# Performance work log

Measured on AMD Instinct MI355X. Metric: run time of the kernel, lower is better.

Reference implementation:

```python
import jax, jax.numpy as jnp
import numpy as np

B, S, E, H = 512, 100, 256, 256
C_EXPLORE = 10.0  # tanh_exploration


def setup_inputs() -> dict:
    key = jax.random.key(0)
    ks = jax.random.split(key, 22)
    sH = 1.0 / np.sqrt(H)
    sE = 1.0 / np.sqrt(E)
    u = lambda k, shp, s: jax.random.uniform(k, shp, minval=-s, maxval=s, dtype=jnp.float32)
    return {
        "inputs": jax.random.uniform(ks[0], (B, 2, S), dtype=jnp.float32),  # 2D coords in [0,1)
        "emb": u(ks[1], (2, E), sE),
        "enc_Wih": u(ks[2], (4 * H, E), sH), "enc_Whh": u(ks[3], (4 * H, H), sH),
        "enc_bih": u(ks[4], (4 * H,), sH), "enc_bhh": u(ks[5], (4 * H,), sH),
        "dec_Wih": u(ks[6], (4 * H, E), sH), "dec_Whh": u(ks[7], (4 * H, H), sH),
        "dec_bih": u(ks[8], (4 * H,), sH), "dec_bhh": u(ks[9], (4 * H,), sH),
        "g_Wq": u(ks[10], (H, H), sH), "g_bq": u(ks[11], (H,), sH),
        "g_Wr": u(ks[12], (H, H), sH), "g_br": u(ks[13], (H,), sH),
        "g_V": u(ks[14], (H,), sH),
        "p_Wq": u(ks[15], (H, H), sH), "p_bq": u(ks[16], (H,), sH),
        "p_Wr": u(ks[17], (H, H), sH), "p_br": u(ks[18], (H,), sH),
        "p_V": u(ks[19], (H,), sH),
        "start": u(ks[20], (E,), sE),
    }


def _lstm_cell(x, h, c, Wih, Whh, bih, bhh):
    # torch LSTM gate order: input, forget, cell, output
    g = x @ Wih.T + h @ Whh.T + bih + bhh
    i, f, gg, o = jnp.split(g, 4, axis=-1)
    c = jax.nn.sigmoid(f) * c + jax.nn.sigmoid(i) * jnp.tanh(gg)
    return jax.nn.sigmoid(o) * jnp.tanh(c), c


def _forward(inputs, emb, enc_Wih, enc_Whh, enc_bih, enc_bhh,
             dec_Wih, dec_Whh, dec_bih, dec_bhh,
             g_Wq, g_bq, g_Wr, g_br, g_V,
             p_Wq, p_bq, p_Wr, p_br, p_V, start):
    # GraphEmbedding: per-position bmm([B,1,2],[B,2,E]) == single einsum
    embedded = jnp.einsum('bcs,ce->bse', inputs, emb)  # [B,S,E]

    h0 = jnp.zeros((B, H), jnp.float32)
    c0 = jnp.zeros((B, H), jnp.float32)

    def enc_step(carry, x_t):
        h, c = carry
        h, c = _lstm_cell(x_t, h, c, enc_Wih, enc_Whh, enc_bih, enc_bhh)
        return (h, c), h

    (h, c), outs = jax.lax.scan(enc_step, (h0, c0), embedded.transpose(1, 0, 2))
    enc = outs.transpose(1, 0, 2)  # encoder_outputs [B,S,H]

    # Conv1d(k=1) projection of encoder outputs is step-invariant: precompute once.
    ref_g = jnp.einsum('bsh,oh->bso', enc, g_Wr) + g_br  # [B,S,H]
    ref_p = jnp.einsum('bsh,oh->bso', enc, p_Wr) + p_br  # [B,S,H]

    keys = jax.random.split(jax.random.key(1), S)
    arange_b = jnp.arange(B)

    def attn(q, ref_proj, Wq, bq, V):
        qq = q @ Wq.T + bq  # [B,H]
        return jnp.einsum('h,bsh->bs', V, jnp.tanh(qq[:, None, :] + ref_proj))

    def step(carry, k):
        h, c, mask, idxs, valid, dec_in = carry
        h, c = _lstm_cell(dec_in, h, c, dec_Wih, dec_Whh, dec_bih, dec_bhh)
        # apply_mask_to_logits: mask grows by idxs only after first selection
        mask = jnp.where(valid, mask.at[arange_b, idxs].set(True), mask)
        # glimpse (n_glimpses = 1, use_tanh=False)
        lg = jnp.where(mask, -jnp.inf, attn(h, ref_g, g_Wq, g_bq, g_V))
        q = jnp.einsum('bsh,bs->bh', enc, jax.nn.softmax(lg, axis=-1))
        # pointer (use_tanh=True, C=10)
        lp = C_EXPLORE * jnp.tanh(attn(q, ref_p, p_Wq, p_bq, p_V))
        lp = jnp.where(mask, -jnp.inf, lp)
        probs = jax.nn.softmax(lp, axis=-1)
        idxs = jax.random.categorical(k, lp)  # multinomial(probs, 1)
        dec_in = embedded[arange_b, idxs]
        return (h, c, mask, idxs, jnp.array(True), dec_in), (probs, idxs)

    init = (h, c, jnp.zeros((B, S), bool), jnp.zeros((B,), jnp.int32),
            jnp.array(False), jnp.broadcast_to(start, (B, E)))
    _, (probs, idxs) = jax.lax.scan(step, init, keys)
    return probs, idxs  # [S,B,S] float, [S,B] int


def reference(inputs, emb, enc_Wih, enc_Whh, enc_bih, enc_bhh,
              dec_Wih, dec_Whh, dec_bih, dec_bhh,
              g_Wq, g_bq, g_Wr, g_br, g_V,
              p_Wq, p_bq, p_Wr, p_br, p_V, start):
    return _forward(inputs, emb, enc_Wih, enc_Whh, enc_bih, enc_bhh,
                    dec_Wih, dec_Whh, dec_bih, dec_bhh,
                    g_Wq, g_bq, g_Wr, g_br, g_V,
                    p_Wq, p_bq, p_Wr, p_br, p_V, start)
```

## Files before the change

### kernel.cpp

```cpp
#include <hip/hip_runtime.h>
#include <cstdint>
#include <math.h>

#define B_ 512
#define S_ 100
#define E_ 256
#define H_ 256

__device__ __forceinline__ float sigmoidf_(float x){ return 1.0f/(1.0f+expf(-x)); }

__device__ __forceinline__ void threefry2x32_(uint32_t k0, uint32_t k1,
                                              uint32_t c0, uint32_t c1,
                                              uint32_t& o0, uint32_t& o1){
  uint32_t ks2 = k0 ^ k1 ^ 0x1BD11BDAu;
  uint32_t x0 = c0 + k0, x1 = c1 + k1;
#define ROT_(x,d) (((x)<<(d))|((x)>>(32-(d))))
#define RND_(r) { x0 += x1; x1 = ROT_(x1,(r)); x1 ^= x0; }
  RND_(13) RND_(15) RND_(26) RND_(6)  x0 += k1;  x1 += ks2 + 1u;
  RND_(17) RND_(29) RND_(16) RND_(24) x0 += ks2; x1 += k0  + 2u;
  RND_(13) RND_(15) RND_(26) RND_(6)  x0 += k0;  x1 += k1  + 3u;
  RND_(17) RND_(29) RND_(16) RND_(24) x0 += k1;  x1 += ks2 + 4u;
  RND_(13) RND_(15) RND_(26) RND_(6)  x0 += ks2; x1 += k0  + 5u;
#undef RND_
#undef ROT_
  o0 = x0; o1 = x1;
}

__device__ __forceinline__ float gumbel_bits_(uint32_t bits){
  const float tiny = 1.175494350822287508e-38f;
  float u = __uint_as_float((bits >> 9) | 0x3f800000u) - 1.0f;
  u = fmaxf(tiny, u + tiny);
  return -logf(-logf(u));
}

__device__ __forceinline__ float wsum_(float v){
  #pragma unroll
  for (int d = 32; d > 0; d >>= 1) v += __shfl_xor(v, d, 64);
  return v;
}
__device__ __forceinline__ float wmax_(float v){
  #pragma unroll
  for (int d = 32; d > 0; d >>= 1) v = fmaxf(v, __shfl_xor(v, d, 64));
  return v;
}

__global__ __launch_bounds__(256) void prep_wt(const float* __restrict__ Wih,
                                               const float* __restrict__ Whh,
                                               float* __restrict__ Wt){
  int idx = blockIdx.x*256 + threadIdx.x;
  int k = idx >> 10, j = idx & 1023;
  Wt[idx] = (k < 256) ? Wih[j*256 + k] : Whh[j*256 + (k-256)];
}
__global__ __launch_bounds__(256) void prep_bias(const float* __restrict__ b1,
                                                 const float* __restrict__ b2,
                                                 float* __restrict__ o, int n){
  int i = blockIdx.x*256 + threadIdx.x; if (i < n) o[i] = b1[i] + b2[i];
}
__global__ __launch_bounds__(256) void transpose256(const float* __restrict__ src,
                                                    float* __restrict__ dst){
  int idx = blockIdx.x*256 + threadIdx.x;
  int r = idx >> 8, cc = idx & 255;
  dst[idx] = src[cc*256 + r];
}
__global__ __launch_bounds__(256) void init_state(float* __restrict__ h, float* __restrict__ c,
                                                  int* __restrict__ mask, int* __restrict__ sel){
  int i = blockIdx.x*256 + threadIdx.x;
  if (i < B_*H_) { h[i] = 0.f; c[i] = 0.f; }
  if (i < B_*S_) mask[i] = 0;
  if (i < B_)    sel[i]  = -1;
}

__global__ __launch_bounds__(256) void lstm_step_kernel(
    const float* __restrict__ Wt,
    const float* __restrict__ bsum,
    const float* __restrict__ coords,
    const float* __restrict__ emb,
    const float* __restrict__ start,
    const int*   __restrict__ sel,
    float* __restrict__ h, float* __restrict__ c,
    float* __restrict__ enc_out,
    int t, int mode)
{
  const int tid = threadIdx.x;
  const int b0  = blockIdx.x * 4;
  __shared__ float xh[4][512];

  const float e0 = emb[tid], e1 = emb[256 + tid];
  #pragma unroll
  for (int r = 0; r < 4; ++r) {
    const int b = b0 + r;
    float xv;
    if (mode == 0) {
      xv = coords[b*200 + t]*e0 + coords[b*200 + 100 + t]*e1;
    } else {
      int s = sel[b];
      if (s < 0) xv = start[tid];
      else       xv = coords[b*200 + s]*e0 + coords[b*200 + 100 + s]*e1;
    }
    xh[r][tid]       = xv;
    xh[r][256 + tid] = h[b*256 + tid];
  }
  __syncthreads();

  float acc[4][4] = {};
  #pragma unroll 4
  for (int k = 0; k < 512; ++k) {
    const float* wr = Wt + (size_t)k*1024 + tid;
    const float w0 = wr[0], w1 = wr[256], w2 = wr[512], w3 = wr[768];
    #pragma unroll
    for (int r = 0; r < 4; ++r) {
      const float xv = xh[r][k];
      acc[r][0] += xv*w0; acc[r][1] += xv*w1;
      acc[r][2] += xv*w2; acc[r][3] += xv*w3;
    }
  }

  const float bi_ = bsum[tid], bf_ = bsum[256+tid], bg_ = bsum[512+tid], bo_ = bsum[768+tid];
  #pragma unroll
  for (int r = 0; r < 4; ++r) {
    const int b = b0 + r;
    const float gi = acc[r][0] + bi_;
    const float gf = acc[r][1] + bf_;
    const float gg = acc[r][2] + bg_;
    const float go = acc[r][3] + bo_;
    const float cN = sigmoidf_(gf)*c[b*256+tid] + sigmoidf_(gi)*tanhf(gg);
    const float hN = sigmoidf_(go)*tanhf(cN);
    c[b*256 + tid] = cN;
    h[b*256 + tid] = hN;
    if (mode == 0) enc_out[((size_t)b*S_ + t)*H_ + tid] = hN;
  }
}

__global__ __launch_bounds__(256) void gemm_ref(
    const float* __restrict__ A, const float* __restrict__ Bt,
    const float* __restrict__ bias, float* __restrict__ C)
{
  const int tid = threadIdx.x;
  const int m0 = blockIdx.x * 128, n0 = blockIdx.y * 128;
  __shared__ float As[8][128];
  __shared__ float Bs[8][128];
  float acc[8][8] = {};
  const int tx = tid & 15, ty = tid >> 4;

  for (int k0 = 0; k0 < 256; k0 += 8) {
    {
      const int row = tid >> 1, q = tid & 1;
      const float4 av = *(const float4*)(A + (size_t)(m0+row)*256 + k0 + q*4);
      As[q*4+0][row] = av.x; As[q*4+1][row] = av.y;
      As[q*4+2][row] = av.z; As[q*4+3][row] = av.w;
    }
    {
      const int kk = tid >> 5, nq = tid & 31;
      *(float4*)(&Bs[kk][nq*4]) = *(const float4*)(Bt + (size_t)(k0+kk)*256 + n0 + nq*4);
    }
    __syncthreads();
    #pragma unroll
    for (int k = 0; k < 8; ++k) {
      float a[8], bb[8];
      *(float4*)&a[0]  = *(const float4*)&As[k][ty*8];
      *(float4*)&a[4]  = *(const float4*)&As[k][ty*8+4];
      *(float4*)&bb[0] = *(const float4*)&Bs[k][tx*8];
      *(float4*)&bb[4] = *(const float4*)&Bs[k][tx*8+4];
      #pragma unroll
      for (int i = 0; i < 8; ++i)
        #pragma unroll
        for (int j = 0; j < 8; ++j)
          acc[i][j] += a[i]*bb[j];
    }
    __syncthreads();
  }
  #pragma unroll
  for (int i = 0; i < 8; ++i) {
    const int m = m0 + ty*8 + i;
    #pragma unroll
    for (int j = 0; j < 8; j += 4) {
      const int n = n0 + tx*8 + j;
      float4 o;
      o.x = acc[i][j  ] + bias[n  ];
      o.y = acc[i][j+1] + bias[n+1];
      o.z = acc[i][j+2] + bias[n+2];
      o.w = acc[i][j+3] + bias[n+3];
      *(float4*)(C + (size_t)m*256 + n) = o;
    }
  }
}

__global__ __launch_bounds__(256) void attn_step(
    const float* __restrict__ h, const float* __restrict__ enc,
    const float* __restrict__ ref_g, const float* __restrict__ ref_p,
    const float* __restrict__ gWqT, const float* __restrict__ g_bq, const float* __restrict__ g_V,
    const float* __restrict__ pWqT, const float* __restrict__ p_bq, const float* __restrict__ p_V,
    int* __restrict__ mask, int* __restrict__ sel,
    float* __restrict__ probs_out, float* __restrict__ idx_out, int t)
{
  const int b    = blockIdx.x;
  const int tid  = threadIdx.x;
  const int lane = tid & 63;
  const int wv   = tid >> 6;

  __shared__ float hs[256], qqs[256], qs[256], pqs[256];
  __shared__ float gVs[256], pVs[256];
  __shared__ float lg[128], alpha[128], lp[128];

  hs[tid]  = h[b*256 + tid];
  gVs[tid] = g_V[tid];
  pVs[tid] = p_V[tid];
  __syncthreads();

  {
    float a = g_bq[tid];
    for (int k = 0; k < 256; ++k) a += hs[k] * gWqT[k*256 + tid];
    qqs[tid] = a;
  }
  __syncthreads();

  {
    const float* rg = ref_g + (size_t)b*S_*H_;
    const int* mk = mask + b*S_;
    for (int is = 0; is < 25; ++is) {
      const int s = is*4 + wv;
      float p = 0.f;
      #pragma unroll
      for (int j = 0; j < 4; ++j) {
        const int hh = lane + 64*j;
        p += gVs[hh] * tanhf(qqs[hh] + rg[s*256 + hh]);
      }
      p = wsum_(p);
      if (lane == 0) lg[s] = mk[s] ? -INFINITY : p;
    }
  }
  __syncthreads();

  if (wv == 0) {
    const float v0 = lg[lane];
    const float v1 = (lane + 64 < S_) ? lg[lane + 64] : -INFINITY;
    const float m  = wmax_(fmaxf(v0, v1));
    const float e0 = expf(v0 - m);
    const float e1 = (lane + 64 < S_) ? expf(v1 - m) : 0.f;
    const float sm = wsum_(e0 + e1);
    alpha[lane] = e0 / sm;
    if (lane + 64 < S_) alpha[lane + 64] = e1 / sm;
  }
  __syncthreads();

  {
    const float* eb = enc + (size_t)b*S_*H_;
    float a = 0.f;
    for (int s = 0; s < S_; ++s) a += alpha[s] * eb[s*256 + tid];
    qs[tid] = a;
  }
  __syncthreads();

  {
    float a = p_bq[tid];
    for (int k = 0; k < 256; ++k) a += qs[k] * pWqT[k*256 + tid];
    pqs[tid] = a;
  }
  __syncthreads();

  {
    const float* rp = ref_p + (size_t)b*S_*H_;
    const int* mk = mask + b*S_;
    for (int is = 0; is < 25; ++is) {
      const int s = is*4 + wv;
      float p = 0.f;
      #pragma unroll
      for (int j = 0; j < 4; ++j) {
        const int hh = lane + 64*j;
        p += pVs[hh] * tanhf(pqs[hh] + rp[s*256 + hh]);
      }
      p = wsum_(p);
      if (lane == 0) {
        const float v = 10.0f * tanhf(p);
        lp[s] = mk[s] ? -INFINITY : v;
      }
    }
  }
  __syncthreads();

  if (wv == 0) {
    const float v0 = lp[lane];
    const float v1 = (lane + 64 < S_) ? lp[lane + 64] : -INFINITY;
    const float m  = wmax_(fmaxf(v0, v1));
    const float e0 = expf(v0 - m);
    const float e1 = (lane + 64 < S_) ? expf(v1 - m) : 0.f;
    const float sm = wsum_(e0 + e1);
    float* po = probs_out + ((size_t)t*B_ + b)*S_;
    po[lane] = e0 / sm;
    if (lane + 64 < S_) po[lane + 64] = e1 / sm;

    uint32_t k0, k1; threefry2x32_(0u, 1u, 0u, (uint32_t)t, k0, k1);
    uint32_t r0, r1;
    threefry2x32_(k0, k1, 0u, (uint32_t)(b*S_ + lane), r0, r1);
    float z0 = v0 + gumbel_bits_(r0 ^ r1);
    float z1 = -INFINITY;
    if (lane + 64 < S_) {
      uint32_t q0, q1;
      threefry2x32_(k0, k1, 0u, (uint32_t)(b*S_ + lane + 64), q0, q1);
      z1 = v1 + gumbel_bits_(q0 ^ q1);
    }
    float bv; int bi;
    if (z1 > z0) { bv = z1; bi = lane + 64; } else { bv = z0; bi = lane; }
    #pragma unroll
    for (int d = 32; d > 0; d >>= 1) {
      const float ov = __shfl_xor(bv, d, 64);
      const int   oi = __shfl_xor(bi, d, 64);
      if (ov > bv || (ov == bv && oi < bi)) { bv = ov; bi = oi; }
    }
    if (lane == 0) {
      idx_out[t*B_ + b] = (float)bi;
      sel[b] = bi;
      mask[b*S_ + bi] = 1;
    }
  }
}

extern "C" void kernel_launch(void* const* d_in, const int* in_sizes, int n_in,
                              void* d_out, int out_size, void* d_ws, size_t ws_size,
                              hipStream_t stream) {
  (void)in_sizes; (void)n_in; (void)out_size; (void)ws_size;
  const float* inputs = (const float*)d_in[0];
  const float* emb    = (const float*)d_in[1];
  const float* eWih   = (const float*)d_in[2];
  const float* eWhh   = (const float*)d_in[3];
  const float* ebih   = (const float*)d_in[4];
  const float* ebhh   = (const float*)d_in[5];
  const float* dWih   = (const float*)d_in[6];
  const float* dWhh   = (const float*)d_in[7];
  const float* dbih   = (const float*)d_in[8];
  const float* dbhh   = (const float*)d_in[9];
  const float* gWq    = (const float*)d_in[10];
  const float* gbq    = (const float*)d_in[11];
  const float* gWr    = (const float*)d_in[12];
  const float* gbr    = (const float*)d_in[13];
  const float* gV     = (const float*)d_in[14];
  const float* pWq    = (const float*)d_in[15];
  const float* pbq    = (const float*)d_in[16];
  const float* pWr    = (const float*)d_in[17];
  const float* pbr    = (const float*)d_in[18];
  const float* pV     = (const float*)d_in[19];
  const float* start  = (const float*)d_in[20];

  float* ws = (float*)d_ws;
  size_t o = 0;
  float* WtE  = ws + o; o += (size_t)512*1024;
  float* WtD  = ws + o; o += (size_t)512*1024;
  float* bE   = ws + o; o += 1024;
  float* bD   = ws + o; o += 1024;
  float* gWqT = ws + o; o += 65536;
  float* pWqT = ws + o; o += 65536;
  float* gWrT = ws + o; o += 65536;
  float* pWrT = ws + o; o += 65536;
  float* enc  = ws + o; o += (size_t)B_*S_*H_;
  float* refg = ws + o; o += (size_t)B_*S_*H_;
  float* refp = ws + o; o += (size_t)B_*S_*H_;
  float* h    = ws + o; o += (size_t)B_*H_;
  float* c    = ws + o; o += (size_t)B_*H_;
  int* mask   = (int*)(ws + o); o += (size_t)B_*S_;
  int* sel    = (int*)(ws + o); o += B_;

  float* probs = (float*)d_out;
  float* idxo  = probs + (size_t)S_*B_*S_;

  prep_wt<<<2048,256,0,stream>>>(eWih, eWhh, WtE);
  prep_wt<<<2048,256,0,stream>>>(dWih, dWhh, WtD);
  prep_bias<<<4,256,0,stream>>>(ebih, ebhh, bE, 1024);
  prep_bias<<<4,256,0,stream>>>(dbih, dbhh, bD, 1024);
  transpose256<<<256,256,0,stream>>>(gWq, gWqT);
  transpose256<<<256,256,0,stream>>>(pWq, pWqT);
  transpose256<<<256,256,0,stream>>>(gWr, gWrT);
  transpose256<<<256,256,0,stream>>>(pWr, pWrT);
  init_state<<<512,256,0,stream>>>(h, c, mask, sel);

  for (int t = 0; t < S_; ++t)
    lstm_step_kernel<<<128,256,0,stream>>>(WtE, bE, inputs, emb, nullptr, nullptr,
                                           h, c, enc, t, 0);

  gemm_ref<<<dim3(400,2),256,0,stream>>>(enc, gWrT, gbr, refg);
  gemm_ref<<<dim3(400,2),256,0,stream>>>(enc, pWrT, pbr, refp);

  for (int t = 0; t < S_; ++t) {
    lstm_step_kernel<<<128,256,0,stream>>>(WtD, bD, inputs, emb, start, sel,
                                           h, c, nullptr, t, 1);
    attn_step<<<512,256,0,stream>>>(h, enc, refg, refp,
                                    gWqT, gbq, gV, pWqT, pbq, pV,
                                    mask, sel, probs, idxo, t);
  }
}
```

Before: 18.85 ms.

## Split attention into batched matvec kernels and retile LSTM step with interleaved gate weights

The LSTM step kernel is retiled so each block handles 8 batch rows and 64 hidden units, reading gate-interleaved weights as float4 and using double-buffered h to avoid the read/write hazard once multiple blocks share a batch row. The fused per-batch attention kernel, which recomputed query projections with a full 256x256 weight read per batch element, is split into separate matvec kernels that process 4 batch rows per block plus glimpse and pointer kernels. This cuts redundant weight traffic and raises parallelism, at the cost of more kernel launches per decode step and extra global round-trips for the intermediate vectors.

```diff
diff --git a/kernel.cpp b/kernel.cpp
--- a/kernel.cpp
+++ b/kernel.cpp
@@ -44,17 +44,22 @@
   return v;
 }
 
-__global__ __launch_bounds__(256) void prep_wt(const float* __restrict__ Wih,
+__global__ __launch_bounds__(256) void prep_w4(const float* __restrict__ Wih,
                                                const float* __restrict__ Whh,
-                                               float* __restrict__ Wt){
+                                               float* __restrict__ W4){
   int idx = blockIdx.x*256 + threadIdx.x;
-  int k = idx >> 10, j = idx & 1023;
-  Wt[idx] = (k < 256) ? Wih[j*256 + k] : Whh[j*256 + (k-256)];
-}
-__global__ __launch_bounds__(256) void prep_bias(const float* __restrict__ b1,
-                                                 const float* __restrict__ b2,
-                                                 float* __restrict__ o, int n){
-  int i = blockIdx.x*256 + threadIdx.x; if (i < n) o[i] = b1[i] + b2[i];
+  int g = idx & 3, u = (idx >> 2) & 255, k = idx >> 10;
+  int row = g*256 + u;
+  W4[idx] = (k < 256) ? Wih[row*256 + k] : Whh[row*256 + (k-256)];
+}
+__global__ __launch_bounds__(256) void prep_b4(const float* __restrict__ b1,
+                                               const float* __restrict__ b2,
+                                               float* __restrict__ o){
+  int idx = blockIdx.x*256 + threadIdx.x;
+  if (idx < 1024) {
+    int g = idx & 3, u = idx >> 2;
+    o[idx] = b1[g*256 + u] + b2[g*256 + u];
+  }
 }
 __global__ __launch_bounds__(256) void transpose256(const float* __restrict__ src,
                                                     float* __restrict__ dst){
@@ -70,64 +75,206 @@
   if (i < B_)    sel[i]  = -1;
 }
 
-__global__ __launch_bounds__(256) void lstm_step_kernel(
-    const float* __restrict__ Wt,
-    const float* __restrict__ bsum,
+__global__ __launch_bounds__(256) void lstm_step2(
+    const float* __restrict__ W4,
+    const float* __restrict__ b4,
     const float* __restrict__ coords,
     const float* __restrict__ emb,
     const float* __restrict__ start,
     const int*   __restrict__ sel,
-    float* __restrict__ h, float* __restrict__ c,
+    const float* __restrict__ hr,
+    float* __restrict__ hw,
+    float* __restrict__ cst,
     float* __restrict__ enc_out,
     int t, int mode)
 {
   const int tid = threadIdx.x;
-  const int b0  = blockIdx.x * 4;
-  __shared__ float xh[4][512];
-
-  const float e0 = emb[tid], e1 = emb[256 + tid];
-  #pragma unroll
-  for (int r = 0; r < 4; ++r) {
-    const int b = b0 + r;
-    float xv;
-    if (mode == 0) {
-      xv = coords[b*200 + t]*e0 + coords[b*200 + 100 + t]*e1;
+  const int uu  = tid & 63;
+  const int rg  = tid >> 6;
+  const int b0  = (blockIdx.x >> 2) * 8;
+  const int u0  = (blockIdx.x & 3) * 64;
+  __shared__ float Xs[512*8];
+
+  for (int i = tid; i < 4096; i += 256) {
+    const int k = i >> 3, r = i & 7, b = b0 + r;
+    float v;
+    if (k < 256) {
+      if (mode == 0) {
+        v = coords[b*200 + t]*emb[k] + coords[b*200 + 100 + t]*emb[256 + k];
+      } else {
+        const int s = sel[b];
+        if (s < 0) v = start[k];
+        else       v = coords[b*200 + s]*emb[k] + coords[b*200 + 100 + s]*emb[256 + k];
+      }
     } else {
-      int s = sel[b];
-      if (s < 0) xv = start[tid];
-      else       xv = coords[b*200 + s]*e0 + coords[b*200 + 100 + s]*e1;
-    }
-    xh[r][tid]       = xv;
-    xh[r][256 + tid] = h[b*256 + tid];
-  }
-  __syncthreads();
-
-  float acc[4][4] = {};
+      v = hr[b*256 + (k - 256)];
+    }
+    Xs[i] = v;
+  }
+  __syncthreads();
+
+  float a0x=0.f,a0y=0.f,a0z=0.f,a0w=0.f, a1x=0.f,a1y=0.f,a1z=0.f,a1w=0.f;
+  const float* wp = W4 + (size_t)(u0 + uu)*4;
   #pragma unroll 4
   for (int k = 0; k < 512; ++k) {
-    const float* wr = Wt + (size_t)k*1024 + tid;
-    const float w0 = wr[0], w1 = wr[256], w2 = wr[512], w3 = wr[768];
+    const float4 w = *(const float4*)(wp + (size_t)k*1024);
+    const float2 x = *(const float2*)(Xs + k*8 + rg*2);
+    a0x += x.x*w.x; a0y += x.x*w.y; a0z += x.x*w.z; a0w += x.x*w.w;
+    a1x += x.y*w.x; a1y += x.y*w.y; a1z += x.y*w.z; a1w += x.y*w.w;
+  }
+
+  const float4 bb = *(const float4*)(b4 + (u0 + uu)*4);
+  const int u = u0 + uu;
+  {
+    const int b = b0 + rg*2;
+    const float gi = a0x + bb.x, gf = a0y + bb.y, gg = a0z + bb.z, go = a0w + bb.w;
+    const float cN = sigmoidf_(gf)*cst[b*256+u] + sigmoidf_(gi)*tanhf(gg);
+    const float hN = sigmoidf_(go)*tanhf(cN);
+    cst[b*256+u] = cN; hw[b*256+u] = hN;
+    if (mode == 0) enc_out[((size_t)b*S_ + t)*H_ + u] = hN;
+  }
+  {
+    const int b = b0 + rg*2 + 1;
+    const float gi = a1x + bb.x, gf = a1y + bb.y, gg = a1z + bb.z, go = a1w + bb.w;
+    const float cN = sigmoidf_(gf)*cst[b*256+u] + sigmoidf_(gi)*tanhf(gg);
+    const float hN = sigmoidf_(go)*tanhf(cN);
+    cst[b*256+u] = cN; hw[b*256+u] = hN;
+    if (mode == 0) enc_out[((size_t)b*S_ + t)*H_ + u] = hN;
+  }
+}
+
+__global__ __launch_bounds__(256) void matvec_bias(
+    const float* __restrict__ X, const float* __restrict__ WT,
+    const float* __restrict__ bias, float* __restrict__ out)
+{
+  const int tid = threadIdx.x;
+  const int b0 = blockIdx.x * 4;
+  __shared__ float Xs[1024];
+  for (int i = tid; i < 1024; i += 256)
+    Xs[i] = X[(b0 + (i & 3))*256 + (i >> 2)];
+  __syncthreads();
+  float a0 = bias[tid];
+  float a1 = a0, a2 = a0, a3 = a0;
+  #pragma unroll 4
+  for (int k = 0; k < 256; ++k) {
+    const float w = WT[k*256 + tid];
+    const float4 x = *(const float4*)(Xs + k*4);
+    a0 += x.x*w; a1 += x.y*w; a2 += x.z*w; a3 += x.w*w;
+  }
+  out[(b0+0)*256 + tid] = a0;
+  out[(b0+1)*256 + tid] = a1;
+  out[(b0+2)*256 + tid] = a2;
+  out[(b0+3)*256 + tid] = a3;
+}
+
+__global__ __launch_bounds__(256) void glimpse_step(
+    const float* __restrict__ qqIn, const float* __restrict__ enc,
+    const float* __restrict__ ref_g, const float* __restrict__ g_V,
+    const int* __restrict__ mask, float* __restrict__ qOut)
+{
+  const int b = blockIdx.x, tid = threadIdx.x, lane = tid & 63, wv = tid >> 6;
+  __shared__ float qqs[256], gVs[256], lg[128], alpha[128];
+  qqs[tid] = qqIn[b*256 + tid];
+  gVs[tid] = g_V[tid];
+  __syncthreads();
+
+  const float* rg = ref_g + (size_t)b*S_*H_;
+  const int* mk = mask + b*S_;
+  for (int is = 0; is < 25; ++is) {
+    const int s = is*4 + wv;
+    float p = 0.f;
     #pragma unroll
-    for (int r = 0; r < 4; ++r) {
-      const float xv = xh[r][k];
-      acc[r][0] += xv*w0; acc[r][1] += xv*w1;
-      acc[r][2] += xv*w2; acc[r][3] += xv*w3;
-    }
-  }
-
-  const float bi_ = bsum[tid], bf_ = bsum[256+tid], bg_ = bsum[512+tid], bo_ = bsum[768+tid];
-  #pragma unroll
-  for (int r = 0; r < 4; ++r) {
-    const int b = b0 + r;
-    const float gi = acc[r][0] + bi_;
-    const float gf = acc[r][1] + bf_;
-    const float gg = acc[r][2] + bg_;
-    const float go = acc[r][3] + bo_;
-    const float cN = sigmoidf_(gf)*c[b*256+tid] + sigmoidf_(gi)*tanhf(gg);
-    const float hN = sigmoidf_(go)*tanhf(cN);
-    c[b*256 + tid] = cN;
-    h[b*256 + tid] = hN;
-    if (mode == 0) enc_out[((size_t)b*S_ + t)*H_ + tid] = hN;
+    for (int j = 0; j < 4; ++j) {
+      const int hh = lane + 64*j;
+      p += gVs[hh] * tanhf(qqs[hh] + rg[s*256 + hh]);
+    }
+    p = wsum_(p);
+    if (lane == 0) lg[s] = mk[s] ? -INFINITY : p;
+  }
+  __syncthreads();
+
+  if (wv == 0) {
+    const float v0 = lg[lane];
+    const float v1 = (lane + 64 < S_) ? lg[lane + 64] : -INFINITY;
+    const float m  = wmax_(fmaxf(v0, v1));
+    const float e0 = expf(v0 - m);
+    const float e1 = (lane + 64 < S_) ? expf(v1 - m) : 0.f;
+    const float sm = wsum_(e0 + e1);
+    alpha[lane] = e0 / sm;
+    if (lane + 64 < S_) alpha[lane + 64] = e1 / sm;
+  }
+  __syncthreads();
+
+  const float* eb = enc + (size_t)b*S_*H_;
+  float a = 0.f;
+  for (int s = 0; s < S_; ++s) a += alpha[s] * eb[s*256 + tid];
+  qOut[b*256 + tid] = a;
+}
+
+__global__ __launch_bounds__(256) void pointer_step(
+    const float* __restrict__ pqIn, const float* __restrict__ ref_p,
+    const float* __restrict__ p_V,
+    int* __restrict__ mask, int* __restrict__ sel,
+    float* __restrict__ probs_out, float* __restrict__ idx_out, int t)
+{
+  const int b = blockIdx.x, tid = threadIdx.x, lane = tid & 63, wv = tid >> 6;
+  __shared__ float pqs[256], pVs[256], lp[128];
+  pqs[tid] = pqIn[b*256 + tid];
+  pVs[tid] = p_V[tid];
+  __syncthreads();
+
+  const float* rp = ref_p + (size_t)b*S_*H_;
+  const int* mk = mask + b*S_;
+  for (int is = 0; is < 25; ++is) {
+    const int s = is*4 + wv;
+    float p = 0.f;
+    #pragma unroll
+    for (int j = 0; j < 4; ++j) {
+      const int hh = lane + 64*j;
+      p += pVs[hh] * tanhf(pqs[hh] + rp[s*256 + hh]);
+    }
+    p = wsum_(p);
+    if (lane == 0) {
+      const float v = 10.0f * tanhf(p);
+      lp[s] = mk[s] ? -INFINITY : v;
+    }
+  }
+  __syncthreads();
+
+  if (wv == 0) {
+    const float v0 = lp[lane];
+    const float v1 = (lane + 64 < S_) ? lp[lane + 64] : -INFINITY;
+    const float m  = wmax_(fmaxf(v0, v1));
+    const float e0 = expf(v0 - m);
+    const float e1 = (lane + 64 < S_) ? expf(v1 - m) : 0.f;
+    const float sm = wsum_(e0 + e1);
+    float* po = probs_out + ((size_t)t*B_ + b)*S_;
+    po[lane] = e0 / sm;
+    if (lane + 64 < S_) po[lane + 64] = e1 / sm;
+
+    uint32_t k0, k1; threefry2x32_(0u, 1u, 0u, (uint32_t)t, k0, k1);
+    uint32_t r0, r1;
+    threefry2x32_(k0, k1, 0u, (uint32_t)(b*S_ + lane), r0, r1);
+    float z0 = v0 + gumbel_bits_(r0 ^ r1);
+    float z1 = -INFINITY;
+    if (lane + 64 < S_) {
+      uint32_t q0, q1;
+      threefry2x32_(k0, k1, 0u, (uint32_t)(b*S_ + lane + 64), q0, q1);
+      z1 = v1 + gumbel_bits_(q0 ^ q1);
+    }
+    float bv; int bi;
+    if (z1 > z0) { bv = z1; bi = lane + 64; } else { bv = z0; bi = lane; }
+    #pragma unroll
+    for (int d = 32; d > 0; d >>= 1) {
+      const float ov = __shfl_xor(bv, d, 64);
+      const int   oi = __shfl_xor(bi, d, 64);
+      if (ov > bv || (ov == bv && oi < bi)) { bv = ov; bi = oi; }
+    }
+    if (lane == 0) {
+      idx_out[t*B_ + b] = (float)bi;
+      sel[b] = bi;
+      mask[b*S_ + bi] = 1;
+    }
   }
 }
 
@@ -181,136 +328,6 @@
       o.z = acc[i][j+2] + bias[n+2];
       o.w = acc[i][j+3] + bias[n+3];
       *(float4*)(C + (size_t)m*256 + n) = o;
-    }
-  }
-}
-
-__global__ __launch_bounds__(256) void attn_step(
-    const float* __restrict__ h, const float* __restrict__ enc,
-    const float* __restrict__ ref_g, const float* __restrict__ ref_p,
-    const float* __restrict__ gWqT, const float* __restrict__ g_bq, const float* __restrict__ g_V,
-    const float* __restrict__ pWqT, const float* __restrict__ p_bq, const float* __restrict__ p_V,
-    int* __restrict__ mask, int* __restrict__ sel,
-    float* __restrict__ probs_out, float* __restrict__ idx_out, int t)
-{
-  const int b    = blockIdx.x;
-  const int tid  = threadIdx.x;
-  const int lane = tid & 63;
-  const int wv   = tid >> 6;
-
-  __shared__ float hs[256], qqs[256], qs[256], pqs[256];
-  __shared__ float gVs[256], pVs[256];
-  __shared__ float lg[128], alpha[128], lp[128];
-
-  hs[tid]  = h[b*256 + tid];
-  gVs[tid] = g_V[tid];
-  pVs[tid] = p_V[tid];
-  __syncthreads();
-
-  {
-    float a = g_bq[tid];
-    for (int k = 0; k < 256; ++k) a += hs[k] * gWqT[k*256 + tid];
-    qqs[tid] = a;
-  }
-  __syncthreads();
-
-  {
-    const float* rg = ref_g + (size_t)b*S_*H_;
-    const int* mk = mask + b*S_;
-    for (int is = 0; is < 25; ++is) {
-      const int s = is*4 + wv;
-      float p = 0.f;
-      #pragma unroll
-      for (int j = 0; j < 4; ++j) {
-        const int hh = lane + 64*j;
-        p += gVs[hh] * tanhf(qqs[hh] + rg[s*256 + hh]);
-      }
-      p = wsum_(p);
-      if (lane == 0) lg[s] = mk[s] ? -INFINITY : p;
-    }
-  }
-  __syncthreads();
-
-  if (wv == 0) {
-    const float v0 = lg[lane];
-    const float v1 = (lane + 64 < S_) ? lg[lane + 64] : -INFINITY;
-    const float m  = wmax_(fmaxf(v0, v1));
-    const float e0 = expf(v0 - m);
-    const float e1 = (lane + 64 < S_) ? expf(v1 - m) : 0.f;
-    const float sm = wsum_(e0 + e1);
-    alpha[lane] = e0 / sm;
-    if (lane + 64 < S_) alpha[lane + 64] = e1 / sm;
-  }
-  __syncthreads();
-
-  {
-    const float* eb = enc + (size_t)b*S_*H_;
-    float a = 0.f;
-    for (int s = 0; s < S_; ++s) a += alpha[s] * eb[s*256 + tid];
-    qs[tid] = a;
-  }
-  __syncthreads();
-
-  {
-    float a = p_bq[tid];
-    for (int k = 0; k < 256; ++k) a += qs[k] * pWqT[k*256 + tid];
-    pqs[tid] = a;
-  }
-  __syncthreads();
-
-  {
-    const float* rp = ref_p + (size_t)b*S_*H_;
-    const int* mk = mask + b*S_;
-    for (int is = 0; is < 25; ++is) {
-      const int s = is*4 + wv;
-      float p = 0.f;
-      #pragma unroll
-      for (int j = 0; j < 4; ++j) {
-        const int hh = lane + 64*j;
-        p += pVs[hh] * tanhf(pqs[hh] + rp[s*256 + hh]);
-      }
-      p = wsum_(p);
-      if (lane == 0) {
-        const float v = 10.0f * tanhf(p);
-        lp[s] = mk[s] ? -INFINITY : v;
-      }
-    }
-  }
-  __syncthreads();
-
-  if (wv == 0) {
-    const float v0 = lp[lane];
-    const float v1 = (lane + 64 < S_) ? lp[lane + 64] : -INFINITY;
-    const float m  = wmax_(fmaxf(v0, v1));
-    const float e0 = expf(v0 - m);
-    const float e1 = (lane + 64 < S_) ? expf(v1 - m) : 0.f;
-    const float sm = wsum_(e0 + e1);
-    float* po = probs_out + ((size_t)t*B_ + b)*S_;
-    po[lane] = e0 / sm;
-    if (lane + 64 < S_) po[lane + 64] = e1 / sm;
-
-    uint32_t k0, k1; threefry2x32_(0u, 1u, 0u, (uint32_t)t, k0, k1);
-    uint32_t r0, r1;
-    threefry2x32_(k0, k1, 0u, (uint32_t)(b*S_ + lane), r0, r1);
-    float z0 = v0 + gumbel_bits_(r0 ^ r1);
-    float z1 = -INFINITY;
-    if (lane + 64 < S_) {
-      uint32_t q0, q1;
-      threefry2x32_(k0, k1, 0u, (uint32_t)(b*S_ + lane + 64), q0, q1);
-      z1 = v1 + gumbel_bits_(q0 ^ q1);
-    }
-    float bv; int bi;
-    if (z1 > z0) { bv = z1; bi = lane + 64; } else { bv = z0; bi = lane; }
-    #pragma unroll
-    for (int d = 32; d > 0; d >>= 1) {
-      const float ov = __shfl_xor(bv, d, 64);
-      const int   oi = __shfl_xor(bi, d, 64);
-      if (ov > bv || (ov == bv && oi < bi)) { bv = ov; bi = oi; }
-    }
-    if (lane == 0) {
-      idx_out[t*B_ + b] = (float)bi;
-      sel[b] = bi;
-      mask[b*S_ + bi] = 1;
     }
   }
 }
@@ -343,10 +360,10 @@
 
   float* ws = (float*)d_ws;
   size_t o = 0;
-  float* WtE  = ws + o; o += (size_t)512*1024;
-  float* WtD  = ws + o; o += (size_t)512*1024;
-  float* bE   = ws + o; o += 1024;
-  float* bD   = ws + o; o += 1024;
+  float* W4E  = ws + o; o += (size_t)512*1024;
+  float* W4D  = ws + o; o += (size_t)512*1024;
+  float* b4E  = ws + o; o += 1024;
+  float* b4D  = ws + o; o += 1024;
   float* gWqT = ws + o; o += 65536;
   float* pWqT = ws + o; o += 65536;
   float* gWrT = ws + o; o += 65536;
@@ -354,36 +371,47 @@
   float* enc  = ws + o; o += (size_t)B_*S_*H_;
   float* refg = ws + o; o += (size_t)B_*S_*H_;
   float* refp = ws + o; o += (size_t)B_*S_*H_;
-  float* h    = ws + o; o += (size_t)B_*H_;
+  float* h0   = ws + o; o += (size_t)B_*H_;
+  float* h1   = ws + o; o += (size_t)B_*H_;
   float* c    = ws + o; o += (size_t)B_*H_;
+  float* qq   = ws + o; o += (size_t)B_*H_;
+  float* qb   = ws + o; o += (size_t)B_*H_;
+  float* pq   = ws + o; o += (size_t)B_*H_;
   int* mask   = (int*)(ws + o); o += (size_t)B_*S_;
   int* sel    = (int*)(ws + o); o += B_;
 
   float* probs = (float*)d_out;
   float* idxo  = probs + (size_t)S_*B_*S_;
 
-  prep_wt<<<2048,256,0,stream>>>(eWih, eWhh, WtE);
-  prep_wt<<<2048,256,0,stream>>>(dWih, dWhh, WtD);
-  prep_bias<<<4,256,0,stream>>>(ebih, ebhh, bE, 1024);
-  prep_bias<<<4,256,0,stream>>>(dbih, dbhh, bD, 1024);
+  float* hpp[2] = {h0, h1};
+  int p = 0;
+
+  prep_w4<<<2048,256,0,stream>>>(eWih, eWhh, W4E);
+  prep_w4<<<2048,256,0,stream>>>(dWih, dWhh, W4D);
+  prep_b4<<<4,256,0,stream>>>(ebih, ebhh, b4E);
+  prep_b4<<<4,256,0,stream>>>(dbih, dbhh, b4D);
   transpose256<<<256,256,0,stream>>>(gWq, gWqT);
   transpose256<<<256,256,0,stream>>>(pWq, pWqT);
   transpose256<<<256,256,0,stream>>>(gWr, gWrT);
   transpose256<<<256,256,0,stream>>>(pWr, pWrT);
-  init_state<<<512,256,0,stream>>>(h, c, mask, sel);
-
-  for (int t = 0; t < S_; ++t)
-    lstm_step_kernel<<<128,256,0,stream>>>(WtE, bE, inputs, emb, nullptr, nullptr,
-                                           h, c, enc, t, 0);
+  init_state<<<512,256,0,stream>>>(h0, c, mask, sel);
+
+  for (int t = 0; t < S_; ++t) {
+    lstm_step2<<<256,256,0,stream>>>(W4E, b4E, inputs, emb, nullptr, nullptr,
+                                     hpp[p], hpp[1-p], c, enc, t, 0);
+    p ^= 1;
+  }
 
   gemm_ref<<<dim3(400,2),256,0,stream>>>(enc, gWrT, gbr, refg);
   gemm_ref<<<dim3(400,2),256,0,stream>>>(enc, pWrT, pbr, refp);
 
   for (int t = 0; t < S_; ++t) {
-    lstm_step_kernel<<<128,256,0,stream>>>(WtD, bD, inputs, emb, start, sel,
-                                           h, c, nullptr, t, 1);
-    attn_step<<<512,256,0,stream>>>(h, enc, refg, refp,
-                                    gWqT, gbq, gV, pWqT, pbq, pV,
-                                    mask, sel, probs, idxo, t);
-  }
-}
+    lstm_step2<<<256,256,0,stream>>>(W4D, b4D, inputs, emb, start, sel,
+                                     hpp[p], hpp[1-p], c, nullptr, t, 1);
+    p ^= 1;
+    matvec_bias<<<128,256,0,stream>>>(hpp[p], gWqT, gbq, qq);
+    glimpse_step<<<512,256,0,stream>>>(qq, enc, refg, gV, mask, qb);
+    matvec_bias<<<128,256,0,stream>>>(qb, pWqT, pbq, pq);
+    pointer_step<<<512,256,0,stream>>>(pq, refp, pV, mask, sel, probs, idxo, t);
+  }
+}
```

After: 22.27 ms. 18.2% more time.
